# Kernel optimization log

Hardware: AMD Instinct MI355X
Metric: run time of the kernel (lower is better)

## Reference

```python
import jax, jax.numpy as jnp
import numpy as np

B, F_, E = 16384, 39, 16
VOCAB_PER = 26000
SUM_FD = F_ * VOCAB_PER
P = F_ * (F_ - 1) // 2  # 741
IN_DIM = F_ * (F_ - 1) + P  # 2223
LMBD = 1.0
LR = 1e-3
STEPS = 1
ROW, COL = np.triu_indices(F_, 1)


def setup_inputs() -> dict:
    key = jax.random.key(0)
    ks = jax.random.split(key, 12)
    x = jax.random.randint(ks[0], (B, F_), 0, VOCAB_PER, dtype=jnp.int64) if jax.config.jax_enable_x64 else jax.random.randint(ks[0], (B, F_), 0, VOCAB_PER)
    emb_b = float(np.sqrt(6.0 / (SUM_FD + E)))
    emb_weight = jax.random.uniform(ks[1], (SUM_FD, E), jnp.float32, -emb_b, emb_b)
    lin_b = float(np.sqrt(6.0 / (SUM_FD + 1)))
    lin_weight = jax.random.uniform(ks[2], (SUM_FD, 1), jnp.float32, -lin_b, lin_b)
    w0 = jnp.full((F_, F_), 1.0 / (F_ - 1), jnp.float32)
    w0 = w0 * (1 - jnp.eye(F_)) - jnp.eye(F_)
    k_b = float(np.sqrt(6.0 / (E + E)))
    kernel = jax.random.uniform(ks[3], (P, E, E), jnp.float32, -k_b, k_b)
    fc1_w = jax.random.normal(ks[4], (100, IN_DIM), jnp.float32) * 0.02
    fc2_w = jax.random.normal(ks[5], (100, 100), jnp.float32) * 0.05
    fc3_w = jax.random.normal(ks[6], (1, 100), jnp.float32) * 0.05
    return {
        'x': x, 'emb_weight': emb_weight, 'lin_weight': lin_weight,
        'w0': w0, 'kernel': kernel,
        'bn1_g': jnp.ones((IN_DIM,), jnp.float32), 'bn1_b': jnp.zeros((IN_DIM,), jnp.float32),
        'fc1_w': fc1_w, 'fc1_b': jnp.zeros((100,), jnp.float32),
        'bn2_g': jnp.ones((100,), jnp.float32), 'bn2_b': jnp.zeros((100,), jnp.float32),
        'fc2_w': fc2_w, 'fc2_b': jnp.zeros((100,), jnp.float32),
        'fc3_w': fc3_w, 'fc3_b': jnp.zeros((1,), jnp.float32),
    }


def _sparse_proj(z):
    # sparsemax-style projection onto the simplex scaled by LMBD; z: [B, F]
    z_s = -jnp.sort(-z, axis=1)          # descending sort
    z0 = z_s[:, :1]
    z = z - z0
    z_s = z_s - z0
    cs = jnp.cumsum(z_s, axis=1)
    taus = (cs - LMBD) / jnp.arange(1, F_ + 1, dtype=z.dtype)
    k = jnp.sum(z_s > taus, axis=1, keepdims=True)
    tau = jnp.take_along_axis(taus, k - 1, axis=1)
    return jax.nn.relu(z - tau)


def _bn(h, g, b):
    m = h.mean(0)
    v = h.var(0)  # biased variance, matching torch BN normalization
    return (h - m) * jax.lax.rsqrt(v + 1e-5) * g + b


def reference(x, emb_weight, lin_weight, w0, kernel, bn1_g, bn1_b,
              fc1_w, fc1_b, bn2_g, bn2_b, fc2_w, fc2_b, fc3_w, fc3_b):
    offsets = jnp.arange(F_, dtype=x.dtype) * VOCAB_PER
    idx = x + offsets[None, :]           # [B, F]
    vx = emb_weight[idx]                 # [B, F, E]
    bsz = vx.shape[0]
    eye = jnp.eye(F_, dtype=vx.dtype)
    w = jnp.broadcast_to(w0, (bsz, F_, F_))
    mu = jnp.full((bsz, F_), LMBD / F_, dtype=vx.dtype)
    wv = jnp.einsum('bij,bje->bie', w, vx)
    for _ in range(STEPS):
        dw = jnp.einsum('bie,bje->bij', wv, vx)          # wv @ vx^T
        dw = (mu / LMBD)[:, :, None] * dw
        w = w - LR * dw
        w = w * (1 - eye) - eye                           # diagonal := -1
        wv = jnp.einsum('bij,bje->bie', w, vx)
        dmu = 0.5 * jnp.sum(wv * wv, axis=2)
        mu = _sparse_proj(mu - LR * dmu)
    # pairwise kernel interaction over upper-triangular field pairs
    ox = jnp.einsum('bpe,pef->bpf', vx[:, ROW, :], kernel)
    ox = jnp.einsum('bpf,bpf->bp', ox, vx[:, COL, :])     # [B, P]
    w = mu[:, :, None] * w
    # strip diagonal: [B,F,F] -> [B, F*(F-1)]
    woff = w.reshape(bsz, F_ * F_)[:, 1:].reshape(bsz, F_ - 1, F_ + 1)[:, :, :-1]
    h = jnp.concatenate([woff.reshape(bsz, -1), ox], axis=1)  # [B, IN_DIM]
    h = jax.nn.relu(_bn(h, bn1_g, bn1_b) @ fc1_w.T + fc1_b)
    h = jax.nn.relu(_bn(h, bn2_g, bn2_b) @ fc2_w.T + fc2_b)
    out = (h @ fc3_w.T + fc3_b)[:, 0]                     # [B]
    lin = jnp.sum(lin_weight[idx][:, :, 0], axis=-1)      # [B]
    return out + lin
```

## Files before the change

### kernel.cpp

```cpp
#include <hip/hip_runtime.h>

#define NB     16384
#define NF     39
#define NE     16
#define VOCAB  26000
#define NP     741
#define NWOFF  1482
#define KDIM   780
#define KPAD   784
#define NUNIT  380

#define OFF_HT    0LL
#define OFF_LIN   6422528LL
#define OFF_ST    6438912LL
#define OFF_UT    6440704LL
#define OFF_W1FT  6442240LL
#define OFF_B1F   6492416LL
#define OFF_W2F   6492544LL
#define OFF_B2F   6502544LL
#define OFF_H2    6502656LL
#define OFF_VX    8337664LL

typedef __attribute__((ext_vector_type(8)))  short short8;
typedef __attribute__((ext_vector_type(4)))  float f32x4;
typedef __attribute__((ext_vector_type(16))) float f32x16;

__device__ __forceinline__ float dot4f(float4 a, float4 b) {
    return fmaf(a.x, b.x, fmaf(a.y, b.y, fmaf(a.z, b.z, a.w * b.w)));
}
__device__ __forceinline__ unsigned short f2bf(float x) {
    unsigned u = __float_as_uint(x);
    unsigned r = ((u >> 16) & 1u) + 0x7FFFu;
    return (unsigned short)((u + r) >> 16);
}
__device__ __forceinline__ float bf2f(unsigned short b) {
    return __uint_as_float(((unsigned)b) << 16);
}

__global__ __launch_bounds__(256, 4) void k_meta(
    const int* __restrict__ x, const float* __restrict__ emb,
    const float* __restrict__ linw, float* __restrict__ ws)
{
    __shared__ float vxt[4][16 * 41];
    __shared__ float Ss[4][16];
    __shared__ int   idxs[4][40];
    __shared__ float part[80];

    const int tid = threadIdx.x;
    const int wv  = tid >> 6;
    const int ln  = tid & 63;

    unsigned short* hT  = (unsigned short*)(ws + OFF_HT);
    unsigned short* vxG = (unsigned short*)(ws + OFF_VX);
    float* lin = ws + OFF_LIN;
    float* mus = ws + OFF_ST;

    const float ALPHA = 1.0f / 38.0f;
    const float CA    = 1.0f + ALPHA;

    if (tid < 80) part[tid] = 0.f;
    __syncthreads();

    float accS = 0.f, accQ = 0.f;
    unsigned short mub[8];

    #pragma unroll
    for (int t = 0; t < 8; ++t) {
        const int b = blockIdx.x * 32 + wv * 8 + t;
        if (ln < 39) idxs[wv][ln] = x[b * 39 + ln] + ln * VOCAB;
        __builtin_amdgcn_wave_barrier();

        float lv = (ln < 39) ? linw[idxs[wv][ln]] : 0.f;

        #pragma unroll
        for (int it = 0; it < 3; ++it) {
            int tt = it * 64 + ln;
            if (tt < 156) {
                int f = tt >> 2, q = tt & 3;
                float4 v = ((const float4*)(emb + (long long)idxs[wv][f] * 16))[q];
                vxt[wv][(q * 4 + 0) * 41 + f] = v.x;
                vxt[wv][(q * 4 + 1) * 41 + f] = v.y;
                vxt[wv][(q * 4 + 2) * 41 + f] = v.z;
                vxt[wv][(q * 4 + 3) * 41 + f] = v.w;
                uint2 pw;
                pw.x = (unsigned)f2bf(v.x) | ((unsigned)f2bf(v.y) << 16);
                pw.y = (unsigned)f2bf(v.z) | ((unsigned)f2bf(v.w) << 16);
                *(uint2*)(vxG + ((size_t)b * 39 + f) * 16 + q * 4) = pw;
            }
        }
        #pragma unroll
        for (int m = 32; m; m >>= 1) lv += __shfl_xor(lv, m, 64);
        if (ln == 0) lin[b] = lv;
        __builtin_amdgcn_wave_barrier();

        if (ln < 16) {
            float s = 0.f;
            const float* row = &vxt[wv][ln * 41];
            #pragma unroll
            for (int j = 0; j < 39; ++j) s += row[j];
            Ss[wv][ln] = s;
        }
        __builtin_amdgcn_wave_barrier();

        float qv = 0.f;
        if (ln < 39) {
            #pragma unroll
            for (int e = 0; e < 16; ++e) {
                float o = ALPHA * Ss[wv][e] - CA * vxt[wv][e * 41 + ln];
                qv = fmaf(o, o, qv);
            }
        }
        float qz = qv;
        #pragma unroll
        for (int m = 32; m; m >>= 1) qz += __shfl_xor(qz, m, 64);
        float hval = fmaf(-5e-4f, qv, (5e-4f / 39.0f) * qz);
        unsigned short mb = f2bf(hval);
        mub[t] = mb;
        if (ln < 39) {
            float mq = bf2f(mb);
            accS += mq; accQ = fmaf(mq, mq, accQ);
        }
        __builtin_amdgcn_wave_barrier();
    }
    if (ln < 39) {
        const int bbase = blockIdx.x * 32 + wv * 8;
        uint4 w;
        w.x = (unsigned)mub[0] | ((unsigned)mub[1] << 16);
        w.y = (unsigned)mub[2] | ((unsigned)mub[3] << 16);
        w.z = (unsigned)mub[4] | ((unsigned)mub[5] << 16);
        w.w = (unsigned)mub[6] | ((unsigned)mub[7] << 16);
        *(uint4*)(hT + (size_t)ln * NB + bbase) = w;
        atomicAdd(&part[ln], accS);
        atomicAdd(&part[40 + ln], accQ);
    }
    if (tid < 128) {
        int c = 780 + (tid >> 5), b = blockIdx.x * 32 + (tid & 31);
        hT[(size_t)c * NB + b] = 0;
    }
    __syncthreads();
    if (tid < 39) {
        atomicAdd(&mus[tid], part[tid]);
        atomicAdd(&mus[40 + tid], part[40 + tid]);
    }
}

__global__ void k_pack(const float* __restrict__ kern, float* __restrict__ ws)
{
    int t = blockIdx.x * 256 + threadIdx.x;
    if (t >= NUNIT * 64) return;
    int u = t >> 6, l = t & 63;

    int i = 0, ustart = 0;
    for (;; ++i) {
        int gsz = (39 - i) >> 1;
        if (ustart + gsz > u) break;
        ustart += gsz;
    }
    int pstart = i * 38 - (i * (i - 1)) / 2;
    int within = u - ustart;
    int p0 = pstart + 2 * within;
    int gcount = 38 - i;
    bool has2 = (2 * within + 1) < gcount;
    int p1 = has2 ? p0 + 1 : p0;
    int j0 = i + 1 + (p0 - pstart);
    int j1 = i + 1 + (p1 - pstart);
    if (l == 0) {
        int4 mt; mt.x = i | (has2 ? 0x100 : 0); mt.y = j0; mt.z = j1; mt.w = p0;
        ((int4*)(ws + OFF_UT))[u] = mt;
    }

    const int m = l & 31, s = m >> 4, f = m & 15, kb = (l >> 5) * 8;
    const int ps = s ? p1 : p0;
    const bool real = s ? has2 : true;
    unsigned short v[8];
    #pragma unroll
    for (int jj = 0; jj < 8; ++jj) {
        float val = real ? kern[ps * 256 + (kb + jj) * 16 + f] : 0.f;
        v[jj] = f2bf(val);
    }
    uint4 w;
    w.x = (unsigned)v[0] | ((unsigned)v[1] << 16);
    w.y = (unsigned)v[2] | ((unsigned)v[3] << 16);
    w.z = (unsigned)v[4] | ((unsigned)v[5] << 16);
    w.w = (unsigned)v[6] | ((unsigned)v[7] << 16);
    ((uint4*)(ws + OFF_H2))[(size_t)u * 64 + l] = w;
}

__global__ __launch_bounds__(256, 3) void k_ox(float* __restrict__ ws)
{
    __shared__ unsigned short vxs[32 * 648];

    const int tid = threadIdx.x;
    const int b0  = blockIdx.x * 32;
    unsigned short* hT = (unsigned short*)(ws + OFF_HT);
    const unsigned short* vxG = (const unsigned short*)(ws + OFF_VX);
    const int4* ut = (const int4*)(ws + OFF_UT);
    const uint4* apk = (const uint4*)(ws + OFF_H2);

    for (int t = tid; t < 2496; t += 256) {
        int row = t / 78, ch = t - row * 78;
        uint4 w = *(const uint4*)(vxG + (size_t)(b0 + row) * 624 + ch * 8);
        *(uint4*)(vxs + row * 648 + ch * 8) = w;
    }
    __syncthreads();

    const int l  = tid & 63;
    const int wv = tid >> 6;
    const int c  = l & 31;
    const int h  = l >> 5;
    const unsigned short* vrow = vxs + c * 648;

    const int uend = blockIdx.y * 190 + 190;
    int u = blockIdx.y * 190 + wv;

    int i_cur = -1;
    short8 bfrag = {0,0,0,0,0,0,0,0};

    int4 mt; uint4 araw;
    if (u < uend) {
        mt = ut[u];
        araw = apk[(size_t)u * 64 + l];
    }

    for (; u < uend; u += 4) {
        int4 mt_n; uint4 araw_n;
        const int un = u + 4;
        if (un < uend) {
            mt_n = ut[un];
            araw_n = apk[(size_t)un * 64 + l];
        }

        const int iw = __builtin_amdgcn_readfirstlane(mt.x);
        const int j0 = __builtin_amdgcn_readfirstlane(mt.y);
        const int j1 = __builtin_amdgcn_readfirstlane(mt.z);
        const int p0 = __builtin_amdgcn_readfirstlane(mt.w);
        const int ig = iw & 0xff;
        const int has2 = iw >> 8;

        if (ig != i_cur) {
            i_cur = ig;
            bfrag = *(const short8*)(vrow + ig * 16 + h * 8);
        }
        short8 af;
        af[0] = (short)(araw.x & 0xffff); af[1] = (short)(araw.x >> 16);
        af[2] = (short)(araw.y & 0xffff); af[3] = (short)(araw.y >> 16);
        af[4] = (short)(araw.z & 0xffff); af[5] = (short)(araw.z >> 16);
        af[6] = (short)(araw.w & 0xffff); af[7] = (short)(araw.w >> 16);

        f32x16 D = {};
        D = __builtin_amdgcn_mfma_f32_32x32x16_bf16(af, bfrag, D, 0, 0, 0);

        ushort4 a0 = *(const ushort4*)(vrow + j0 * 16 + 4 * h);
        ushort4 a1 = *(const ushort4*)(vrow + j0 * 16 + 8 + 4 * h);
        ushort4 a2 = *(const ushort4*)(vrow + j1 * 16 + 4 * h);
        ushort4 a3 = *(const ushort4*)(vrow + j1 * 16 + 8 + 4 * h);

        float g0 = fmaf(bf2f(a0.y), D[1],  bf2f(a0.x) * D[0]);
        float g1 = fmaf(bf2f(a0.w), D[3],  bf2f(a0.z) * D[2]);
        float g2 = fmaf(bf2f(a1.y), D[5],  bf2f(a1.x) * D[4]);
        float g3 = fmaf(bf2f(a1.w), D[7],  bf2f(a1.z) * D[6]);
        float s0 = (g0 + g1) + (g2 + g3);

        float e0 = fmaf(bf2f(a2.y), D[9],  bf2f(a2.x) * D[8]);
        float e1 = fmaf(bf2f(a2.w), D[11], bf2f(a2.z) * D[10]);
        float e2 = fmaf(bf2f(a3.y), D[13], bf2f(a3.x) * D[12]);
        float e3 = fmaf(bf2f(a3.w), D[15], bf2f(a3.z) * D[14]);
        float s1 = (e0 + e1) + (e2 + e3);

        s0 += __shfl_xor(s0, 32, 64);
        s1 += __shfl_xor(s1, 32, 64);

        unsigned short outv = h ? f2bf(s1) : f2bf(s0);
        if (h == 0 || has2)
            hT[(size_t)(39 + p0 + h) * NB + b0 + c] = outv;

        mt = mt_n; araw = araw_n;
    }
}

__global__ __launch_bounds__(256) void k_stats(float* __restrict__ ws)
{
    __shared__ float rs[4], rq[4];
    const unsigned short* hT = (const unsigned short*)(ws + OFF_HT);
    const int tid = threadIdx.x;
    const int p = blockIdx.x;
    const uint4* col = (const uint4*)(hT + (size_t)(39 + p) * NB);
    float s = 0.f, q = 0.f;
    #pragma unroll
    for (int it = 0; it < 8; ++it) {
        uint4 v = col[it * 256 + tid];
        unsigned wds[4] = {v.x, v.y, v.z, v.w};
        #pragma unroll
        for (int w = 0; w < 4; ++w) {
            float lo = bf2f((unsigned short)(wds[w] & 0xffff));
            float hi = bf2f((unsigned short)(wds[w] >> 16));
            s += lo + hi;
            q = fmaf(lo, lo, q); q = fmaf(hi, hi, q);
        }
    }
    #pragma unroll
    for (int m = 32; m; m >>= 1) { s += __shfl_xor(s, m, 64); q += __shfl_xor(q, m, 64); }
    if ((tid & 63) == 0) { rs[tid >> 6] = s; rq[tid >> 6] = q; }
    __syncthreads();
    if (tid == 0) {
        (ws + OFF_ST + 80)[p]  = rs[0] + rs[1] + rs[2] + rs[3];
        (ws + OFF_ST + 824)[p] = rq[0] + rq[1] + rq[2] + rq[3];
    }
}

__global__ void k_fold1(const float* __restrict__ fc1w, const float* __restrict__ g1,
                        const float* __restrict__ b1v, const float* __restrict__ fc1b,
                        float* __restrict__ ws)
{
    __shared__ float red[4];
    const float* st = ws + OFF_ST;
    const float ALPHA = 1.0f / 38.0f;
    const int tid = threadIdx.x;

    if (blockIdx.x < 392) {
        int e = blockIdx.x * 256 + tid;
        if (e >= KPAD * 128) return;
        int r = e >> 7, o = e & 127;
        float val = 0.f;
        if (o < 100 && r < KDIM) {
            if (r < 39) {
                int i = r;
                float m = st[i] * (1.0f / 16384.0f);
                float v = st[40 + i] * (1.0f / 16384.0f) - m * m;
                float Ri = rsqrtf(ALPHA * ALPHA * v + 1e-5f);
                float acc = 0.f;
                for (int j = 0; j < 39; ++j) {
                    if (j == i) continue;
                    int n = 39 * i + j;
                    int k = ((n - 1) / 40) * 39 + (n - 1) % 40;
                    acc = fmaf(g1[k], fc1w[o * 2223 + k], acc);
                }
                val = ALPHA * Ri * acc;
            } else {
                int p = r - 39;
                int cidx = NWOFF + p;
                float m = st[80 + p] * (1.0f / 16384.0f);
                float v = st[824 + p] * (1.0f / 16384.0f) - m * m;
                float sc = g1[cidx] * rsqrtf(v + 1e-5f);
                val = fc1w[o * 2223 + cidx] * sc;
            }
        }
        int ks = r >> 4, kk = r & 15, q = kk >> 3, j = kk & 7;
        int nt = o >> 5, lane = q * 32 + (o & 31);
        ((unsigned short*)(ws + OFF_W1FT))[(((size_t)ks * 4 + nt) * 64 + lane) * 8 + j] = f2bf(val);
    } else {
        const int o = blockIdx.x - 392;
        float acc = 0.f;
        for (int k = tid; k < 2223; k += 256) {
            float mean, sc;
            if (k < NWOFF) {
                int n = k + k / 39 + 1;
                int i = n / 39;
                float m = st[i] * (1.0f / 16384.0f);
                float v = st[40 + i] * (1.0f / 16384.0f) - m * m;
                float Ri = rsqrtf(ALPHA * ALPHA * v + 1e-5f);
                mean = ALPHA * m;
                sc = g1[k] * Ri;
            } else {
                int p = k - NWOFF;
                float m = st[80 + p] * (1.0f / 16384.0f);
                float v = st[824 + p] * (1.0f / 16384.0f) - m * m;
                mean = m;
                sc = g1[k] * rsqrtf(v + 1e-5f);
            }
            acc += fc1w[(long long)o * 2223 + k] * (b1v[k] - mean * sc);
        }
        #pragma unroll
        for (int m = 32; m; m >>= 1) acc += __shfl_xor(acc, m, 64);
        if ((tid & 63) == 0) red[tid >> 6] = acc;
        __syncthreads();
        if (tid == 0) (ws + OFF_B1F)[o] = fc1b[o] + red[0] + red[1] + red[2] + red[3];
    }
}

__global__ __launch_bounds__(256, 2) void k_gemm1(float* __restrict__ ws)
{
    __shared__ unsigned short As[2][32 * 116];
    __shared__ float colsum[128], colsq[128], b1s[128];

    const int tid = threadIdx.x;
    const size_t b0 = (size_t)blockIdx.x * 32;
    const unsigned short* hT = (const unsigned short*)(ws + OFF_HT);
    const unsigned short* wpk = (const unsigned short*)(ws + OFF_W1FT);
    const float* b1f = ws + OFF_B1F;
    float* h2    = ws + OFF_H2;
    float* gsum2 = ws + OFF_ST + 1568;
    float* gsq2  = ws + OFF_ST + 1672;

    if (tid < 128) {
        colsum[tid] = 0.f; colsq[tid] = 0.f;
        b1s[tid] = (tid < 100) ? b1f[tid] : 0.f;
    }

    const int tk0 = tid >> 2, tseg0 = tid & 3;
    const int t1 = tid + 256;
    const int tk1 = t1 >> 2, tseg1 = t1 & 3;

    {
        uint4 v = *(const uint4*)(hT + (size_t)tk0 * NB + b0 + tseg0 * 8);
        unsigned short* d = As[0] + (tseg0 * 8) * 116 + tk0;
        d[0*116] = (unsigned short)(v.x & 0xffff); d[1*116] = (unsigned short)(v.x >> 16);
        d[2*116] = (unsigned short)(v.y & 0xffff); d[3*116] = (unsigned short)(v.y >> 16);
        d[4*116] = (unsigned short)(v.z & 0xffff); d[5*116] = (unsigned short)(v.z >> 16);
        d[6*116] = (unsigned short)(v.w & 0xffff); d[7*116] = (unsigned short)(v.w >> 16);
        if (t1 < 448) {
            uint4 w = *(const uint4*)(hT + (size_t)tk1 * NB + b0 + tseg1 * 8);
            unsigned short* e = As[0] + (tseg1 * 8) * 116 + tk1;
            e[0*116] = (unsigned short)(w.x & 0xffff); e[1*116] = (unsigned short)(w.x >> 16);
            e[2*116] = (unsigned short)(w.y & 0xffff); e[3*116] = (unsigned short)(w.y >> 16);
            e[4*116] = (unsigned short)(w.z & 0xffff); e[5*116] = (unsigned short)(w.z >> 16);
            e[6*116] = (unsigned short)(w.w & 0xffff); e[7*116] = (unsigned short)(w.w >> 16);
        }
    }
    __syncthreads();

    const int l  = tid & 63;
    const int wn = tid >> 6;
    const int lm = l & 31;
    const int q  = l >> 5;

    f32x16 Da = {}, Db = {};

    for (int ch = 0; ch < 7; ++ch) {
        const int cur = ch & 1;
        uint4 pf0, pf1;
        const bool hn = (ch + 1 < 7);
        if (hn) {
            const int kb = (ch + 1) * 112;
            pf0 = *(const uint4*)(hT + (size_t)(kb + tk0) * NB + b0 + tseg0 * 8);
            if (t1 < 448)
                pf1 = *(const uint4*)(hT + (size_t)(kb + tk1) * NB + b0 + tseg1 * 8);
        }
        const unsigned short* abase = As[cur] + lm * 116 + q * 8;
        #pragma unroll
        for (int ks = 0; ks < 7; ++ks) {
            const unsigned short* pa = abase + ks * 16;
            ushort4 alo = *(const ushort4*)(pa);
            ushort4 ahi = *(const ushort4*)(pa + 4);
            short8 af;
            af[0] = (short)alo.x; af[1] = (short)alo.y;
            af[2] = (short)alo.z; af[3] = (short)alo.w;
            af[4] = (short)ahi.x; af[5] = (short)ahi.y;
            af[6] = (short)ahi.z; af[7] = (short)ahi.w;
            const int kstep = ch * 7 + ks;
            short8 bf = *(const short8*)(wpk + (((size_t)kstep * 4 + wn) * 64 + l) * 8);
            if (ks & 1) Db = __builtin_amdgcn_mfma_f32_32x32x16_bf16(af, bf, Db, 0, 0, 0);
            else        Da = __builtin_amdgcn_mfma_f32_32x32x16_bf16(af, bf, Da, 0, 0, 0);
        }
        if (hn) {
            unsigned short* d = As[cur ^ 1] + (tseg0 * 8) * 116 + tk0;
            d[0*116] = (unsigned short)(pf0.x & 0xffff); d[1*116] = (unsigned short)(pf0.x >> 16);
            d[2*116] = (unsigned short)(pf0.y & 0xffff); d[3*116] = (unsigned short)(pf0.y >> 16);
            d[4*116] = (unsigned short)(pf0.z & 0xffff); d[5*116] = (unsigned short)(pf0.z >> 16);
            d[6*116] = (unsigned short)(pf0.w & 0xffff); d[7*116] = (unsigned short)(pf0.w >> 16);
            if (t1 < 448) {
                unsigned short* e = As[cur ^ 1] + (tseg1 * 8) * 116 + tk1;
                e[0*116] = (unsigned short)(pf1.x & 0xffff); e[1*116] = (unsigned short)(pf1.x >> 16);
                e[2*116] = (unsigned short)(pf1.y & 0xffff); e[3*116] = (unsigned short)(pf1.y >> 16);
                e[4*116] = (unsigned short)(pf1.z & 0xffff); e[5*116] = (unsigned short)(pf1.z >> 16);
                e[6*116] = (unsigned short)(pf1.w & 0xffff); e[7*116] = (unsigned short)(pf1.w >> 16);
            }
        }
        __syncthreads();
    }

    const int c = wn * 32 + lm;
    float bias = (c < 100) ? b1s[c] : 0.f;
    float s = 0.f, qq = 0.f;
    if (c < 100) {
        #pragma unroll
        for (int r = 0; r < 16; ++r) {
            int m = (r & 3) + 8 * (r >> 2) + 4 * q;
            float v = fmaxf((Da[r] + Db[r]) + bias, 0.f);
            h2[(b0 + m) * 112 + c] = v;
            s += v; qq = fmaf(v, v, qq);
        }
        atomicAdd(&colsum[c], s);
        atomicAdd(&colsq[c], qq);
    }
    __syncthreads();
    if (tid < 100) {
        atomicAdd(&gsum2[tid], colsum[tid]);
        atomicAdd(&gsq2[tid],  colsq[tid]);
    }
}

__global__ void k_fold2(const float* __restrict__ fc2w, const float* __restrict__ fc2b,
                        const float* __restrict__ g2, const float* __restrict__ b2,
                        float* __restrict__ ws)
{
    __shared__ float red[2];
    const int o = blockIdx.x, tid = threadIdx.x;
    const float* gsum2 = ws + OFF_ST + 1568;
    const float* gsq2  = ws + OFF_ST + 1672;
    float* W2f = ws + OFF_W2F;
    float acc = 0.f;
    if (tid < 100) {
        float mean = gsum2[tid] * (1.0f / 16384.0f);
        float var  = gsq2[tid] * (1.0f / 16384.0f) - mean * mean;
        float sc   = g2[tid] * rsqrtf(var + 1e-5f);
        float sh   = b2[tid] - mean * sc;
        float w    = fc2w[o * 100 + tid];
        W2f[o * 100 + tid] = w * sc;
        acc = w * sh;
    }
    #pragma unroll
    for (int m = 32; m; m >>= 1) acc += __shfl_xor(acc, m, 64);
    if (tid == 0)  red[0] = acc;
    if (tid == 64) red[1] = acc;
    __syncthreads();
    if (tid == 0) (ws + OFF_B2F)[o] = fc2b[o] + red[0] + red[1];
}

__global__ __launch_bounds__(256) void k_final(
    const float* __restrict__ fc3w, const float* __restrict__ fc3b,
    const float* __restrict__ ws, float* __restrict__ out)
{
    alignas(16) __shared__ float h2s[64 * 108];
    __shared__ float W2s[100 * 100];
    __shared__ float f3s[100], b2s[100];

    const int tid = threadIdx.x;
    const long long b0 = (long long)blockIdx.x * 64;
    const float* h2  = ws + OFF_H2;
    const float* W2f = ws + OFF_W2F;
    const float* b2f = ws + OFF_B2F;
    const float* lin = ws + OFF_LIN;

    if (tid < 100) { f3s[tid] = fc3w[tid]; b2s[tid] = b2f[tid]; }
    for (int t = tid; t < 6400; t += 256) {
        int r2 = t / 100, c = t - r2 * 100;
        h2s[r2 * 108 + c] = h2[(b0 + r2) * 112 + c];
    }
    for (int t = tid; t < 10000; t += 256) W2s[t] = W2f[t];
    __syncthreads();

    const int r = tid >> 2, q = tid & 3;
    const float4* hrow = (const float4*)(h2s + r * 108);
    float acc = 0.f;
    for (int oi = 0; oi < 25; ++oi) {
        int o = q * 25 + oi;
        const float4* wr = (const float4*)(W2s + o * 100);
        float d = 0.f;
        #pragma unroll
        for (int c4 = 0; c4 < 25; ++c4) d += dot4f(hrow[c4], wr[c4]);
        d += b2s[o];
        d = d > 0.f ? d : 0.f;
        acc = fmaf(f3s[o], d, acc);
    }
    acc += __shfl_xor(acc, 1, 64);
    acc += __shfl_xor(acc, 2, 64);
    if (q == 0) out[b0 + r] = acc + fc3b[0] + lin[b0 + r];
}

extern "C" void kernel_launch(void* const* d_in, const int* in_sizes, int n_in,
                              void* d_out, int out_size, void* d_ws, size_t ws_size,
                              hipStream_t stream)
{
    (void)in_sizes; (void)n_in; (void)out_size; (void)ws_size;
    const int*   x    = (const int*)d_in[0];
    const float* emb  = (const float*)d_in[1];
    const float* linw = (const float*)d_in[2];
    const float* kern = (const float*)d_in[4];
    const float* g1   = (const float*)d_in[5];
    const float* b1   = (const float*)d_in[6];
    const float* fc1w = (const float*)d_in[7];
    const float* fc1b = (const float*)d_in[8];
    const float* g2   = (const float*)d_in[9];
    const float* b2   = (const float*)d_in[10];
    const float* fc2w = (const float*)d_in[11];
    const float* fc2b = (const float*)d_in[12];
    const float* fc3w = (const float*)d_in[13];
    const float* fc3b = (const float*)d_in[14];
    float* ws  = (float*)d_ws;
    float* out = (float*)d_out;

    hipMemsetAsync(ws + OFF_ST, 0, 1776 * sizeof(float), stream);
    k_meta  <<<512, 256, 0, stream>>>(x, emb, linw, ws);
    k_pack  <<<95,  256, 0, stream>>>(kern, ws);
    k_ox    <<<dim3(512, 2), 256, 0, stream>>>(ws);
    k_stats <<<741, 256, 0, stream>>>(ws);
    k_fold1 <<<492, 256, 0, stream>>>(fc1w, g1, b1, fc1b, ws);
    k_gemm1 <<<512, 256, 0, stream>>>(ws);
    k_fold2 <<<100, 128, 0, stream>>>(fc2w, fc2b, g2, b2, ws);
    k_final <<<256, 256, 0, stream>>>(fc3w, fc3b, ws, out);
}
```

Before: 286.0 us.

## Fuse BN column statistics into k_ox via atomics and deepen prefetch

```diff
diff --git a/kernel.cpp b/kernel.cpp
--- a/kernel.cpp
+++ b/kernel.cpp
@@ -20,6 +20,8 @@
 #define OFF_B2F   6502544LL
 #define OFF_H2    6502656LL
 #define OFF_VX    8337664LL
+
+#define VSTR   628
 
 typedef __attribute__((ext_vector_type(8)))  short short8;
 typedef __attribute__((ext_vector_type(4)))  float f32x4;
@@ -186,9 +188,9 @@
     ((uint4*)(ws + OFF_H2))[(size_t)u * 64 + l] = w;
 }
 
-__global__ __launch_bounds__(256, 3) void k_ox(float* __restrict__ ws)
-{
-    __shared__ unsigned short vxs[32 * 648];
+__global__ __launch_bounds__(256, 4) void k_ox(float* __restrict__ ws)
+{
+    __shared__ unsigned short vxs[32 * VSTR];
 
     const int tid = threadIdx.x;
     const int b0  = blockIdx.x * 32;
@@ -196,11 +198,17 @@
     const unsigned short* vxG = (const unsigned short*)(ws + OFF_VX);
     const int4* ut = (const int4*)(ws + OFF_UT);
     const uint4* apk = (const uint4*)(ws + OFF_H2);
+    float* oxsum = ws + OFF_ST + 80;
+    float* oxsq  = ws + OFF_ST + 824;
 
     for (int t = tid; t < 2496; t += 256) {
         int row = t / 78, ch = t - row * 78;
         uint4 w = *(const uint4*)(vxG + (size_t)(b0 + row) * 624 + ch * 8);
-        *(uint4*)(vxs + row * 648 + ch * 8) = w;
+        unsigned short* dp = vxs + row * VSTR + ch * 8;
+        uint2 d0; d0.x = w.x; d0.y = w.y;
+        uint2 d1; d1.x = w.z; d1.y = w.w;
+        *(uint2*)(dp)     = d0;
+        *(uint2*)(dp + 4) = d1;
     }
     __syncthreads();
 
@@ -208,47 +216,44 @@
     const int wv = tid >> 6;
     const int c  = l & 31;
     const int h  = l >> 5;
-    const unsigned short* vrow = vxs + c * 648;
+    const unsigned short* vrow = vxs + c * VSTR;
 
     const int uend = blockIdx.y * 190 + 190;
     int u = blockIdx.y * 190 + wv;
 
     int i_cur = -1;
     short8 bfrag = {0,0,0,0,0,0,0,0};
-
-    int4 mt; uint4 araw;
-    if (u < uend) {
-        mt = ut[u];
-        araw = apk[(size_t)u * 64 + l];
-    }
+    const f32x16 Z = {};
+
+    int4 mt_c = {0,0,0,0}, mt_n = {0,0,0,0};
+    uint4 ar_c = {0,0,0,0}, ar_n = {0,0,0,0};
+    if (u < uend)     { mt_c = ut[u];     ar_c = apk[(size_t)u * 64 + l]; }
+    if (u + 4 < uend) { mt_n = ut[u + 4]; ar_n = apk[(size_t)(u + 4) * 64 + l]; }
 
     for (; u < uend; u += 4) {
-        int4 mt_n; uint4 araw_n;
-        const int un = u + 4;
-        if (un < uend) {
-            mt_n = ut[un];
-            araw_n = apk[(size_t)un * 64 + l];
-        }
-
-        const int iw = __builtin_amdgcn_readfirstlane(mt.x);
-        const int j0 = __builtin_amdgcn_readfirstlane(mt.y);
-        const int j1 = __builtin_amdgcn_readfirstlane(mt.z);
-        const int p0 = __builtin_amdgcn_readfirstlane(mt.w);
+        int4 mt_f = {0,0,0,0}; uint4 ar_f = {0,0,0,0};
+        const int uf = u + 8;
+        if (uf < uend) { mt_f = ut[uf]; ar_f = apk[(size_t)uf * 64 + l]; }
+
+        const int iw = __builtin_amdgcn_readfirstlane(mt_c.x);
+        const int j0 = __builtin_amdgcn_readfirstlane(mt_c.y);
+        const int j1 = __builtin_amdgcn_readfirstlane(mt_c.z);
+        const int p0 = __builtin_amdgcn_readfirstlane(mt_c.w);
         const int ig = iw & 0xff;
         const int has2 = iw >> 8;
 
         if (ig != i_cur) {
             i_cur = ig;
-            bfrag = *(const short8*)(vrow + ig * 16 + h * 8);
-        }
-        short8 af;
-        af[0] = (short)(araw.x & 0xffff); af[1] = (short)(araw.x >> 16);
-        af[2] = (short)(araw.y & 0xffff); af[3] = (short)(araw.y >> 16);
-        af[4] = (short)(araw.z & 0xffff); af[5] = (short)(araw.z >> 16);
-        af[6] = (short)(araw.w & 0xffff); af[7] = (short)(araw.w >> 16);
-
-        f32x16 D = {};
-        D = __builtin_amdgcn_mfma_f32_32x32x16_bf16(af, bfrag, D, 0, 0, 0);
+            const uint2* bp = (const uint2*)(vrow + ig * 16 + h * 8);
+            uint2 blo = bp[0], bhi = bp[1];
+            union { uint4 u4; short8 s8; } bc;
+            bc.u4.x = blo.x; bc.u4.y = blo.y; bc.u4.z = bhi.x; bc.u4.w = bhi.y;
+            bfrag = bc.s8;
+        }
+        union { uint4 u4; short8 s8; } ac;
+        ac.u4 = ar_c;
+
+        f32x16 D = __builtin_amdgcn_mfma_f32_32x32x16_bf16(ac.s8, bfrag, Z, 0, 0, 0);
 
         ushort4 a0 = *(const ushort4*)(vrow + j0 * 16 + 4 * h);
         ushort4 a1 = *(const ushort4*)(vrow + j0 * 16 + 8 + 4 * h);
@@ -271,40 +276,24 @@
         s1 += __shfl_xor(s1, 32, 64);
 
         unsigned short outv = h ? f2bf(s1) : f2bf(s0);
-        if (h == 0 || has2)
+        const bool valid = (h == 0) || (has2 != 0);
+        if (valid)
             hT[(size_t)(39 + p0 + h) * NB + b0 + c] = outv;
 
-        mt = mt_n; araw = araw_n;
-    }
-}
-
-__global__ __launch_bounds__(256) void k_stats(float* __restrict__ ws)
-{
-    __shared__ float rs[4], rq[4];
-    const unsigned short* hT = (const unsigned short*)(ws + OFF_HT);
-    const int tid = threadIdx.x;
-    const int p = blockIdx.x;
-    const uint4* col = (const uint4*)(hT + (size_t)(39 + p) * NB);
-    float s = 0.f, q = 0.f;
-    #pragma unroll
-    for (int it = 0; it < 8; ++it) {
-        uint4 v = col[it * 256 + tid];
-        unsigned wds[4] = {v.x, v.y, v.z, v.w};
-        #pragma unroll
-        for (int w = 0; w < 4; ++w) {
-            float lo = bf2f((unsigned short)(wds[w] & 0xffff));
-            float hi = bf2f((unsigned short)(wds[w] >> 16));
-            s += lo + hi;
-            q = fmaf(lo, lo, q); q = fmaf(hi, hi, q);
-        }
-    }
-    #pragma unroll
-    for (int m = 32; m; m >>= 1) { s += __shfl_xor(s, m, 64); q += __shfl_xor(q, m, 64); }
-    if ((tid & 63) == 0) { rs[tid >> 6] = s; rq[tid >> 6] = q; }
-    __syncthreads();
-    if (tid == 0) {
-        (ws + OFF_ST + 80)[p]  = rs[0] + rs[1] + rs[2] + rs[3];
-        (ws + OFF_ST + 824)[p] = rq[0] + rq[1] + rq[2] + rq[3];
+        float rv = bf2f(outv);
+        float rq = rv * rv;
+        #pragma unroll
+        for (int m = 1; m <= 16; m <<= 1) {
+            rv += __shfl_xor(rv, m, 64);
+            rq += __shfl_xor(rq, m, 64);
+        }
+        if (c == 0 && valid) {
+            atomicAdd(&oxsum[p0 + h], rv);
+            atomicAdd(&oxsq[p0 + h],  rq);
+        }
+
+        mt_c = mt_n; ar_c = ar_n;
+        mt_n = mt_f; ar_n = ar_f;
     }
 }
 
@@ -584,7 +573,6 @@
     k_meta  <<<512, 256, 0, stream>>>(x, emb, linw, ws);
     k_pack  <<<95,  256, 0, stream>>>(kern, ws);
     k_ox    <<<dim3(512, 2), 256, 0, stream>>>(ws);
-    k_stats <<<741, 256, 0, stream>>>(ws);
     k_fold1 <<<492, 256, 0, stream>>>(fc1w, g1, b1, fc1b, ws);
     k_gemm1 <<<512, 256, 0, stream>>>(ws);
     k_fold2 <<<100, 128, 0, stream>>>(fc2w, fc2b, g2, b2, ws);
```

Measured after the change: 616.1 us. +115.4%, slower.
